# Kernel optimization log

Hardware: AMD Instinct MI355X
Metric: run time of the kernel (lower is better)

The kernel has to match this reference:

```python
import jax, jax.numpy as jnp
import numpy as np

EMBED_DIM = 1024
NUM_HEADS = 16
HEAD_DIM = EMBED_DIM // NUM_HEADS


def setup_inputs() -> dict:
    key = jax.random.key(0)
    ks = jax.random.split(key, 10)
    s = 1.0 / np.sqrt(EMBED_DIM)
    x = jax.random.normal(ks[0], (4, 2048, EMBED_DIM), dtype=jnp.float32)
    return {
        "x": x,
        "Wq": jax.random.normal(ks[1], (EMBED_DIM, EMBED_DIM), jnp.float32) * s,
        "bq": jnp.zeros((EMBED_DIM,), jnp.float32),
        "Wk": jax.random.normal(ks[2], (EMBED_DIM, EMBED_DIM), jnp.float32) * s,
        "bk": jnp.zeros((EMBED_DIM,), jnp.float32),
        "Wv": jax.random.normal(ks[3], (EMBED_DIM, EMBED_DIM), jnp.float32) * s,
        "bv": jnp.zeros((EMBED_DIM,), jnp.float32),
        "Wo": jax.random.normal(ks[4], (EMBED_DIM, EMBED_DIM), jnp.float32) * s,
        "bo": jnp.zeros((EMBED_DIM,), jnp.float32),
        "head_scaling": jnp.ones((NUM_HEADS,), jnp.float32),
    }


def reference(x, Wq, bq, Wk, bk, Wv, bv, Wo, bo, head_scaling):
    B, S, E = x.shape
    H, D = NUM_HEADS, HEAD_DIM
    scale = 1.0 / np.sqrt(D)
    # projections (torch Linear: y = x @ W.T + b)
    q = (x @ Wq.T + bq).reshape(B, S, H, D).transpose(0, 2, 1, 3)  # [B,H,S,D]
    k = (x @ Wk.T + bk).reshape(B, S, H, D).transpose(0, 2, 1, 3)
    v = (x @ Wv.T + bv).reshape(B, S, H, D).transpose(0, 2, 1, 3)
    scores = jnp.einsum("bhqd,bhkd->bhqk", q, k) * scale
    attn = jax.nn.softmax(scores, axis=-1)
    head_imp = jax.nn.softmax(head_scaling)[None, :, None, None]  # [1,H,1,1]
    attn = attn * head_imp
    out = jnp.einsum("bhqk,bhkd->bhqd", attn, v)
    out = out.transpose(0, 2, 1, 3).reshape(B, S, E)
    return out @ Wo.T + bo
```

## Files before the change

### kernel.cpp

```cpp
#include <hip/hip_runtime.h>

typedef __bf16 bf16x8 __attribute__((ext_vector_type(8)));
typedef float f32x4 __attribute__((ext_vector_type(4)));

constexpr int E = 1024;
constexpr int T = 8192;
constexpr size_t TE  = (size_t)T * E;
constexpr size_t WSZ = (size_t)E * E;

#define QSCALE 0.18033688011112042f

__device__ __forceinline__ unsigned short f2bf(float f) {
    union { float f; unsigned int i; } x; x.f = f;
    unsigned int i = x.i;
    return (unsigned short)((i + 0x7fffu + ((i >> 16) & 1u)) >> 16);
}

__device__ __forceinline__ unsigned int pack_rtz(float lo, float hi) {
    return __builtin_amdgcn_perm(
        __builtin_bit_cast(unsigned int, hi),
        __builtin_bit_cast(unsigned int, lo), 0x07060302u);
}

__device__ __forceinline__ void gload16(const unsigned short* g, unsigned short* l) {
    __builtin_amdgcn_global_load_lds(
        (const __attribute__((address_space(1))) unsigned int*)g,
        (__attribute__((address_space(3))) unsigned int*)l, 16, 0, 0);
}

__global__ __launch_bounds__(256)
void cvt_kernel(const float* __restrict__ x,
                const float* __restrict__ w0, const float* __restrict__ w1,
                const float* __restrict__ w2, const float* __restrict__ w3,
                unsigned short* __restrict__ xb, unsigned short* __restrict__ wb)
{
    size_t i = ((size_t)blockIdx.x * 256 + threadIdx.x) * 8;
    const float* src;
    unsigned short* dst;
    if (i < TE) { src = x + i; dst = xb + i; }
    else {
        size_t j = i - TE;
        int w = (int)(j >> 20);
        size_t off = j & (WSZ - 1);
        src = (w == 0 ? w0 : w == 1 ? w1 : w == 2 ? w2 : w3) + off;
        dst = wb + ((size_t)w << 20) + off;
    }
    float4 a = *(const float4*)src;
    float4 b = *(const float4*)(src + 4);
    union { unsigned short u[8]; uint4 v; } p;
    p.u[0] = f2bf(a.x); p.u[1] = f2bf(a.y); p.u[2] = f2bf(a.z); p.u[3] = f2bf(a.w);
    p.u[4] = f2bf(b.x); p.u[5] = f2bf(b.y); p.u[6] = f2bf(b.z); p.u[7] = f2bf(b.w);
    *(uint4*)dst = p.v;
}

template <int MODE>
__device__ __forceinline__ void gemm_body2(unsigned short* __restrict__ As,
                                           unsigned short* __restrict__ Bs,
                                           const unsigned short* __restrict__ X,
                                           const unsigned short* __restrict__ W,
                                           const float* __restrict__ bias,
                                           void* __restrict__ outp, int t0, int n0,
                                           float oscale)
{
    const int tid  = threadIdx.x;
    const int wave = tid >> 6;
    const int lane = tid & 63;
    const int quad = lane >> 4;
    const int l16  = lane & 15;
    const int wm   = wave >> 2;
    const int wn   = wave & 3;
    const int srow = tid >> 3;
    const int sch  = (tid & 7) ^ ((tid >> 4) & 7);
    const int fsw8 = (l16 >> 1) & 7;

    f32x4 acc[4][4];
#pragma unroll
    for (int i = 0; i < 4; i++)
#pragma unroll
        for (int j = 0; j < 4; j++)
            acc[i][j] = (f32x4){0.f, 0.f, 0.f, 0.f};

    for (int k0 = 0; k0 < E; k0 += 64) {
#pragma unroll
        for (int p = 0; p < 2; p++)
            gload16(&X[(size_t)(t0 + p * 64 + srow) * E + k0 + sch * 8], &As[p * 4096 + tid * 8]);
#pragma unroll
        for (int p = 0; p < 4; p++)
            gload16(&W[(size_t)(n0 + p * 64 + srow) * E + k0 + sch * 8], &Bs[p * 4096 + tid * 8]);
        __syncthreads();

#pragma unroll
        for (int ks = 0; ks < 2; ks++) {
            const int rch = ((ks * 4 + quad) ^ fsw8) * 8;
            bf16x8 af[4], bfr[4];
#pragma unroll
            for (int i = 0; i < 4; i++)
                af[i] = *(const bf16x8*)&As[(wm * 64 + i * 16 + l16) * 64 + rch];
#pragma unroll
            for (int j = 0; j < 4; j++)
                bfr[j] = *(const bf16x8*)&Bs[(wn * 64 + j * 16 + l16) * 64 + rch];

#pragma unroll
            for (int i = 0; i < 4; i++)
#pragma unroll
                for (int j = 0; j < 4; j++) {
                    if (MODE == 2)
                        acc[i][j] = __builtin_amdgcn_mfma_f32_16x16x32_bf16(af[i], bfr[j], acc[i][j], 0, 0, 0);
                    else
                        acc[i][j] = __builtin_amdgcn_mfma_f32_16x16x32_bf16(bfr[j], af[i], acc[i][j], 0, 0, 0);
                }
        }
        __syncthreads();
    }

    if (MODE == 2) {
#pragma unroll
        for (int j = 0; j < 4; j++) {
            const int gc = n0 + wn * 64 + j * 16 + l16;
            const float bj = bias[gc];
#pragma unroll
            for (int i = 0; i < 4; i++) {
                const int gr0 = t0 + wm * 64 + i * 16 + quad * 4;
                union { unsigned short u[4]; uint2 v; } o;
#pragma unroll
                for (int r = 0; r < 4; r++) o.u[r] = f2bf((acc[i][j][r] + bj) * oscale);
                unsigned short* vt = (unsigned short*)outp;
                *(uint2*)&vt[((size_t)((gr0 >> 11) * 16 + (gc >> 6)) * 64 + (gc & 63)) * 2048 + (gr0 & 2047)] = o.v;
            }
        }
    } else {
#pragma unroll
        for (int j = 0; j < 4; j++) {
            const int nb = n0 + wn * 64 + j * 16 + quad * 4;
            const float4 b4 = *(const float4*)&bias[nb];
#pragma unroll
            for (int i = 0; i < 4; i++) {
                const int t = t0 + wm * 64 + i * 16 + l16;
                union { unsigned short u[4]; uint2 v; } o;
                o.u[0] = f2bf((acc[i][j][0] + b4.x) * oscale);
                o.u[1] = f2bf((acc[i][j][1] + b4.y) * oscale);
                o.u[2] = f2bf((acc[i][j][2] + b4.z) * oscale);
                o.u[3] = f2bf((acc[i][j][3] + b4.w) * oscale);
                *(uint2*)&((unsigned short*)outp)[(size_t)t * E + nb] = o.v;
            }
        }
    }
}

__device__ __forceinline__ void gemm_body_out(const unsigned short* __restrict__ X,
                                              const unsigned short* __restrict__ W,
                                              const float* __restrict__ bias,
                                              float* __restrict__ outp, int t0, int n0)
{
    __shared__ unsigned short As[128 * 64];
    __shared__ unsigned short Bs[128 * 64];

    const int tid  = threadIdx.x;
    const int wave = tid >> 6;
    const int lane = tid & 63;
    const int quad = lane >> 4;
    const int l16  = lane & 15;
    const int wm   = wave >> 1;
    const int wn   = wave & 1;
    const int srow = tid >> 3;
    const int sch  = (tid & 7) ^ ((tid >> 4) & 7);
    const int fsw8 = (l16 >> 1) & 7;

    f32x4 acc[4][4];
#pragma unroll
    for (int i = 0; i < 4; i++)
#pragma unroll
        for (int j = 0; j < 4; j++)
            acc[i][j] = (f32x4){0.f, 0.f, 0.f, 0.f};

    for (int k0 = 0; k0 < E; k0 += 64) {
#pragma unroll
        for (int j = 0; j < 4; j++) {
            gload16(&X[(size_t)(t0 + j * 32 + srow) * E + k0 + sch * 8], &As[j * 2048 + tid * 8]);
            gload16(&W[(size_t)(n0 + j * 32 + srow) * E + k0 + sch * 8], &Bs[j * 2048 + tid * 8]);
        }
        __syncthreads();

#pragma unroll
        for (int ks = 0; ks < 2; ks++) {
            const int rch = ((ks * 4 + quad) ^ fsw8) * 8;
            bf16x8 af[4], bfr[4];
#pragma unroll
            for (int i = 0; i < 4; i++)
                af[i] = *(const bf16x8*)&As[(wm * 64 + i * 16 + l16) * 64 + rch];
#pragma unroll
            for (int j = 0; j < 4; j++)
                bfr[j] = *(const bf16x8*)&Bs[(wn * 64 + j * 16 + l16) * 64 + rch];

#pragma unroll
            for (int i = 0; i < 4; i++)
#pragma unroll
                for (int j = 0; j < 4; j++)
                    acc[i][j] = __builtin_amdgcn_mfma_f32_16x16x32_bf16(bfr[j], af[i], acc[i][j], 0, 0, 0);
        }
        __syncthreads();
    }

#pragma unroll
    for (int j = 0; j < 4; j++) {
        const int nb = n0 + wn * 64 + j * 16 + quad * 4;
        const float4 b4 = *(const float4*)&bias[nb];
#pragma unroll
        for (int i = 0; i < 4; i++) {
            const int t = t0 + wm * 64 + i * 16 + l16;
            float4 o;
            o.x = acc[i][j][0] + b4.x;
            o.y = acc[i][j][1] + b4.y;
            o.z = acc[i][j][2] + b4.z;
            o.w = acc[i][j][3] + b4.w;
            *(float4*)&outp[(size_t)t * E + nb] = o;
        }
    }
}

__global__ __launch_bounds__(512)
void gemm_qkv(const unsigned short* __restrict__ Xb, const unsigned short* __restrict__ Wb,
              const float* __restrict__ bq, const float* __restrict__ bk, const float* __restrict__ bv,
              unsigned short* __restrict__ Qb, unsigned short* __restrict__ Kb, unsigned short* __restrict__ VTb)
{
    __shared__ unsigned short smem[(128 + 256) * 64];
    unsigned short* As = smem;
    unsigned short* Bs = smem + 128 * 64;

    const int t0 = blockIdx.x * 128;
    const int y = blockIdx.y;
    const int seg = y >> 2;
    const int n0 = (y & 3) * 256;
    const unsigned short* W = Wb + (size_t)seg * WSZ;
    if (seg == 0)      gemm_body2<0>(As, Bs, Xb, W, bq, Qb,  t0, n0, QSCALE);
    else if (seg == 1) gemm_body2<0>(As, Bs, Xb, W, bk, Kb,  t0, n0, 1.0f);
    else               gemm_body2<2>(As, Bs, Xb, W, bv, VTb, t0, n0, 1.0f);
}

__global__ __launch_bounds__(256, 4)
void gemm_out(const unsigned short* __restrict__ AOb, const unsigned short* __restrict__ Wob,
              const float* __restrict__ bo, float* __restrict__ out)
{
    gemm_body_out(AOb, Wob, bo, out, blockIdx.x * 128, blockIdx.y * 128);
}

__global__ __launch_bounds__(256, 4)
void attn_kernel(const unsigned short* __restrict__ Q,
                 const unsigned short* __restrict__ K,
                 const unsigned short* __restrict__ VT,
                 const float* __restrict__ hs,
                 unsigned short* __restrict__ AO)
{
    constexpr int S = 2048, H = 16;
    const int hb = blockIdx.x;
    const int qt = blockIdx.y;
    const int h  = hb >> 2;
    const int b  = hb & 3;

    const int tid  = threadIdx.x;
    const int wave = tid >> 6;
    const int lane = tid & 63;
    const int quad = lane >> 4;
    const int l16  = lane & 15;

    __shared__ unsigned short Kpl[2][2 * 64 * 32];
    __shared__ unsigned short Vpl[2][64 * 64];

    float mx = -1e30f;
    for (int i = 0; i < H; i++) mx = fmaxf(mx, hs[i]);
    float ss = 0.f;
    for (int i = 0; i < H; i++) ss += __expf(hs[i] - mx);
    const float head_imp = __expf(hs[h] - mx) / ss;

    const int base_t  = b * S;
    const int colbase = h * 64;
    const int q0 = qt * 128 + wave * 32;

    bf16x8 qf[2][2];
#pragma unroll
    for (int qi = 0; qi < 2; qi++)
#pragma unroll
        for (int c = 0; c < 2; c++)
            qf[qi][c] = *(const bf16x8*)&Q[(size_t)(base_t + q0 + qi * 16 + l16) * E + colbase + c * 32 + quad * 8];

    union { unsigned short u[8]; bf16x8 v; } onesf;
    {
        const unsigned short ov = (l16 == 0) ? (unsigned short)0x3F80 : (unsigned short)0;
#pragma unroll
        for (int j = 0; j < 8; j++) onesf.u[j] = ov;
    }

    f32x4 oT[2][4];
#pragma unroll
    for (int qi = 0; qi < 2; qi++)
#pragma unroll
        for (int t = 0; t < 4; t++) oT[qi][t] = (f32x4){0.f, 0.f, 0.f, 0.f};
    f32x4 oT5[2];
    oT5[0] = (f32x4){0.f, 0.f, 0.f, 0.f};
    oT5[1] = (f32x4){0.f, 0.f, 0.f, 0.f};

    const int ksc  = (tid & 3) ^ ((tid >> 3) & 3);
    const int vsc  = (tid & 7) ^ ((tid >> 4) & 7);
    const int fsw  = (l16 >> 1) & 3;
    const int fsw8 = (l16 >> 1) & 7;
    const unsigned short* const vbase = VT + (size_t)(b * 16 + h) * 64 * 2048;

    const unsigned short* kg = &K[(size_t)(base_t + (tid >> 2)) * E + colbase + ksc * 8];
    const unsigned short* vg = &vbase[(size_t)(tid >> 3) * 2048 + vsc * 8];

    auto stage = [&](int bu) {
#pragma unroll
        for (int j = 0; j < 2; j++)
            gload16(kg + j * 32, &Kpl[bu][j * 2048 + tid * 8]);
#pragma unroll
        for (int j = 0; j < 2; j++)
            gload16(vg + (size_t)j * 32 * 2048, &Vpl[bu][j * 2048 + tid * 8]);
        kg += 64 * E;
        vg += 64;
    };

    stage(0);

#pragma unroll 2
    for (int kt = 0; kt < 32; kt++) {
        __syncthreads();
        if (kt < 31) stage((kt + 1) & 1);
        const int cb = kt & 1;

        union { unsigned int w[4]; bf16x8 v; } pb[2][2];
#pragma unroll
        for (int ks = 0; ks < 2; ks++) {
            unsigned int pw[2][4];
#pragma unroll
            for (int tkl = 0; tkl < 2; tkl++) {
                const int tk = ks * 2 + tkl;
                const int ko = (tk * 16 + l16) * 32 + (quad ^ fsw) * 8;
                bf16x8 kf0 = *(const bf16x8*)&Kpl[cb][ko];
                bf16x8 kf1 = *(const bf16x8*)&Kpl[cb][2048 + ko];
#pragma unroll
                for (int qi = 0; qi < 2; qi++) {
                    f32x4 st = (f32x4){0.f, 0.f, 0.f, 0.f};
                    st = __builtin_amdgcn_mfma_f32_16x16x32_bf16(kf0, qf[qi][0], st, 0, 0, 0);
                    st = __builtin_amdgcn_mfma_f32_16x16x32_bf16(kf1, qf[qi][1], st, 0, 0, 0);
                    float p0 = __builtin_amdgcn_exp2f(st[0]);
                    float p1 = __builtin_amdgcn_exp2f(st[1]);
                    float p2 = __builtin_amdgcn_exp2f(st[2]);
                    float p3 = __builtin_amdgcn_exp2f(st[3]);
                    pw[qi][tkl * 2 + 0] = pack_rtz(p0, p1);
                    pw[qi][tkl * 2 + 1] = pack_rtz(p2, p3);
                }
            }
#pragma unroll
            for (int qi = 0; qi < 2; qi++) {
                auto s1 = __builtin_amdgcn_permlane32_swap(pw[qi][0], pw[qi][2], false, false);
                auto s2 = __builtin_amdgcn_permlane32_swap(pw[qi][1], pw[qi][3], false, false);
                auto t1 = __builtin_amdgcn_permlane16_swap(s1[0], s1[1], false, false);
                auto t2 = __builtin_amdgcn_permlane16_swap(s2[0], s2[1], false, false);
                pb[qi][ks].w[0] = t1[0];
                pb[qi][ks].w[1] = t2[0];
                pb[qi][ks].w[2] = t1[1];
                pb[qi][ks].w[3] = t2[1];
            }
        }

        __builtin_amdgcn_s_setprio(1);
#pragma unroll
        for (int tau = 0; tau < 4; tau++) {
#pragma unroll
            for (int ks = 0; ks < 2; ks++) {
                bf16x8 vf = *(const bf16x8*)&Vpl[cb][(tau * 16 + l16) * 64 + ((ks * 4 + quad) ^ fsw8) * 8];
#pragma unroll
                for (int qi = 0; qi < 2; qi++)
                    oT[qi][tau] = __builtin_amdgcn_mfma_f32_16x16x32_bf16(vf, pb[qi][ks].v, oT[qi][tau], 0, 0, 0);
            }
        }
#pragma unroll
        for (int qi = 0; qi < 2; qi++)
#pragma unroll
            for (int ks = 0; ks < 2; ks++)
                oT5[qi] = __builtin_amdgcn_mfma_f32_16x16x32_bf16(onesf.v, pb[qi][ks].v, oT5[qi], 0, 0, 0);
        __builtin_amdgcn_s_setprio(0);
    }

#pragma unroll
    for (int qi = 0; qi < 2; qi++) {
        const float l = __shfl(oT5[qi][0], l16);
        const float inv = head_imp / l;
#pragma unroll
        for (int tau = 0; tau < 4; tau++) {
            union { unsigned short u[4]; uint2 v; } o;
#pragma unroll
            for (int r = 0; r < 4; r++) o.u[r] = f2bf(oT[qi][tau][r] * inv);
            *(uint2*)&AO[(size_t)(base_t + q0 + qi * 16 + l16) * E + colbase + tau * 16 + quad * 4] = o.v;
        }
    }
}

extern "C" void kernel_launch(void* const* d_in, const int* in_sizes, int n_in,
                              void* d_out, int out_size, void* d_ws, size_t ws_size,
                              hipStream_t stream)
{
    const float* x  = (const float*)d_in[0];
    const float* Wq = (const float*)d_in[1];
    const float* bq = (const float*)d_in[2];
    const float* Wk = (const float*)d_in[3];
    const float* bk = (const float*)d_in[4];
    const float* Wv = (const float*)d_in[5];
    const float* bv = (const float*)d_in[6];
    const float* Wo = (const float*)d_in[7];
    const float* bo = (const float*)d_in[8];
    const float* hs = (const float*)d_in[9];
    float* out = (float*)d_out;

    unsigned short* ws = (unsigned short*)d_ws;
    unsigned short* xb  = ws;
    unsigned short* wb  = ws + TE;
    unsigned short* Qb  = ws + TE + 4 * WSZ;
    unsigned short* AOb = Qb + TE;

    unsigned short* Kb;
    unsigned short* VTb;
    const size_t need_bytes = (5 * TE + 4 * WSZ) * sizeof(unsigned short);
    if (ws_size >= need_bytes) {
        Kb  = AOb + TE;
        VTb = Kb + TE;
    } else {
        Kb  = (unsigned short*)d_out;
        VTb = Kb + TE;
    }

    hipLaunchKernelGGL(cvt_kernel, dim3(6144, 1, 1), dim3(256, 1, 1), 0, stream, x, Wq, Wk, Wv, Wo, xb, wb);
    hipLaunchKernelGGL(gemm_qkv, dim3(64, 12, 1), dim3(512, 1, 1), 0, stream, xb, wb, bq, bk, bv, Qb, Kb, VTb);
    hipLaunchKernelGGL(attn_kernel, dim3(64, 16, 1), dim3(256, 1, 1), 0, stream, Qb, Kb, VTb, hs, AOb);
    hipLaunchKernelGGL(gemm_out, dim3(64, 8, 1), dim3(256, 1, 1), 0, stream, AOb, wb + 3 * WSZ, bo, out);
}
```

Before: 258.0 us.

## Double-buffer GEMM LDS tiles with K-step 32 and one barrier per iteration

Both projection GEMMs (QKV and output) now use two LDS buffers holding 32-wide K tiles instead of one 64-wide tile. The next tile's global-to-LDS load is issued right after a single barrier, so it overlaps with the MFMA work on the current buffer, and the second barrier per iteration is gone. The swizzle is rewritten for the 4-chunk rows. Trade-offs are twice as many loop iterations with fewer MFMAs per barrier, and a different LDS footprint that may affect occupancy.

```diff
diff --git a/kernel.cpp b/kernel.cpp
--- a/kernel.cpp
+++ b/kernel.cpp
@@ -54,8 +54,7 @@
 }
 
 template <int MODE>
-__device__ __forceinline__ void gemm_body2(unsigned short* __restrict__ As,
-                                           unsigned short* __restrict__ Bs,
+__device__ __forceinline__ void gemm_body2(unsigned short* __restrict__ smem,
                                            const unsigned short* __restrict__ X,
                                            const unsigned short* __restrict__ W,
                                            const float* __restrict__ bias,
@@ -69,9 +68,8 @@
     const int l16  = lane & 15;
     const int wm   = wave >> 2;
     const int wn   = wave & 3;
-    const int srow = tid >> 3;
-    const int sch  = (tid & 7) ^ ((tid >> 4) & 7);
-    const int fsw8 = (l16 >> 1) & 7;
+    const int gc   = (tid & 3) ^ ((tid >> 3) & 3);
+    const int fsw  = (l16 >> 1) & 3;
 
     f32x4 acc[4][4];
 #pragma unroll
@@ -80,44 +78,50 @@
         for (int j = 0; j < 4; j++)
             acc[i][j] = (f32x4){0.f, 0.f, 0.f, 0.f};
 
-    for (int k0 = 0; k0 < E; k0 += 64) {
-#pragma unroll
-        for (int p = 0; p < 2; p++)
-            gload16(&X[(size_t)(t0 + p * 64 + srow) * E + k0 + sch * 8], &As[p * 4096 + tid * 8]);
-#pragma unroll
-        for (int p = 0; p < 4; p++)
-            gload16(&W[(size_t)(n0 + p * 64 + srow) * E + k0 + sch * 8], &Bs[p * 4096 + tid * 8]);
+    const unsigned short* xg = &X[(size_t)(t0 + (tid >> 2)) * E + gc * 8];
+    const unsigned short* wg = &W[(size_t)(n0 + (tid >> 2)) * E + gc * 8];
+
+    auto stage = [&](int bu) {
+        unsigned short* buf = smem + bu * 12288;
+        gload16(xg, &buf[tid * 8]);
+        gload16(wg, &buf[4096 + tid * 8]);
+        gload16(wg + (size_t)128 * E, &buf[8192 + tid * 8]);
+        xg += 32; wg += 32;
+    };
+
+    stage(0);
+
+#pragma unroll 2
+    for (int kt = 0; kt < 32; kt++) {
         __syncthreads();
-
-#pragma unroll
-        for (int ks = 0; ks < 2; ks++) {
-            const int rch = ((ks * 4 + quad) ^ fsw8) * 8;
-            bf16x8 af[4], bfr[4];
-#pragma unroll
-            for (int i = 0; i < 4; i++)
-                af[i] = *(const bf16x8*)&As[(wm * 64 + i * 16 + l16) * 64 + rch];
-#pragma unroll
-            for (int j = 0; j < 4; j++)
-                bfr[j] = *(const bf16x8*)&Bs[(wn * 64 + j * 16 + l16) * 64 + rch];
-
-#pragma unroll
-            for (int i = 0; i < 4; i++)
-#pragma unroll
-                for (int j = 0; j < 4; j++) {
-                    if (MODE == 2)
-                        acc[i][j] = __builtin_amdgcn_mfma_f32_16x16x32_bf16(af[i], bfr[j], acc[i][j], 0, 0, 0);
-                    else
-                        acc[i][j] = __builtin_amdgcn_mfma_f32_16x16x32_bf16(bfr[j], af[i], acc[i][j], 0, 0, 0);
-                }
-        }
-        __syncthreads();
+        if (kt < 31) stage((kt + 1) & 1);
+        const unsigned short* As = smem + (kt & 1) * 12288;
+        const unsigned short* Bs = As + 4096;
+
+        bf16x8 af[4], bfr[4];
+#pragma unroll
+        for (int i = 0; i < 4; i++)
+            af[i] = *(const bf16x8*)&As[(wm * 64 + i * 16 + l16) * 32 + (quad ^ fsw) * 8];
+#pragma unroll
+        for (int j = 0; j < 4; j++)
+            bfr[j] = *(const bf16x8*)&Bs[(wn * 64 + j * 16 + l16) * 32 + (quad ^ fsw) * 8];
+
+#pragma unroll
+        for (int i = 0; i < 4; i++)
+#pragma unroll
+            for (int j = 0; j < 4; j++) {
+                if (MODE == 2)
+                    acc[i][j] = __builtin_amdgcn_mfma_f32_16x16x32_bf16(af[i], bfr[j], acc[i][j], 0, 0, 0);
+                else
+                    acc[i][j] = __builtin_amdgcn_mfma_f32_16x16x32_bf16(bfr[j], af[i], acc[i][j], 0, 0, 0);
+            }
     }
 
     if (MODE == 2) {
 #pragma unroll
         for (int j = 0; j < 4; j++) {
-            const int gc = n0 + wn * 64 + j * 16 + l16;
-            const float bj = bias[gc];
+            const int gcn = n0 + wn * 64 + j * 16 + l16;
+            const float bj = bias[gcn];
 #pragma unroll
             for (int i = 0; i < 4; i++) {
                 const int gr0 = t0 + wm * 64 + i * 16 + quad * 4;
@@ -125,7 +129,7 @@
 #pragma unroll
                 for (int r = 0; r < 4; r++) o.u[r] = f2bf((acc[i][j][r] + bj) * oscale);
                 unsigned short* vt = (unsigned short*)outp;
-                *(uint2*)&vt[((size_t)((gr0 >> 11) * 16 + (gc >> 6)) * 64 + (gc & 63)) * 2048 + (gr0 & 2047)] = o.v;
+                *(uint2*)&vt[((size_t)((gr0 >> 11) * 16 + (gcn >> 6)) * 64 + (gcn & 63)) * 2048 + (gr0 & 2047)] = o.v;
             }
         }
     } else {
@@ -152,8 +156,7 @@
                                               const float* __restrict__ bias,
                                               float* __restrict__ outp, int t0, int n0)
 {
-    __shared__ unsigned short As[128 * 64];
-    __shared__ unsigned short Bs[128 * 64];
+    __shared__ unsigned short smem[2 * (128 + 128) * 32];
 
     const int tid  = threadIdx.x;
     const int wave = tid >> 6;
@@ -162,9 +165,8 @@
     const int l16  = lane & 15;
     const int wm   = wave >> 1;
     const int wn   = wave & 1;
-    const int srow = tid >> 3;
-    const int sch  = (tid & 7) ^ ((tid >> 4) & 7);
-    const int fsw8 = (l16 >> 1) & 7;
+    const int gc   = (tid & 3) ^ ((tid >> 3) & 3);
+    const int fsw  = (l16 >> 1) & 3;
 
     f32x4 acc[4][4];
 #pragma unroll
@@ -173,32 +175,40 @@
         for (int j = 0; j < 4; j++)
             acc[i][j] = (f32x4){0.f, 0.f, 0.f, 0.f};
 
-    for (int k0 = 0; k0 < E; k0 += 64) {
-#pragma unroll
-        for (int j = 0; j < 4; j++) {
-            gload16(&X[(size_t)(t0 + j * 32 + srow) * E + k0 + sch * 8], &As[j * 2048 + tid * 8]);
-            gload16(&W[(size_t)(n0 + j * 32 + srow) * E + k0 + sch * 8], &Bs[j * 2048 + tid * 8]);
-        }
+    const unsigned short* xg = &X[(size_t)(t0 + (tid >> 2)) * E + gc * 8];
+    const unsigned short* wg = &W[(size_t)(n0 + (tid >> 2)) * E + gc * 8];
+
+    auto stage = [&](int bu) {
+        unsigned short* buf = smem + bu * 8192;
+        gload16(xg, &buf[tid * 8]);
+        gload16(xg + (size_t)64 * E, &buf[2048 + tid * 8]);
+        gload16(wg, &buf[4096 + tid * 8]);
+        gload16(wg + (size_t)64 * E, &buf[6144 + tid * 8]);
+        xg += 32; wg += 32;
+    };
+
+    stage(0);
+
+#pragma unroll 2
+    for (int kt = 0; kt < 32; kt++) {
         __syncthreads();
-
-#pragma unroll
-        for (int ks = 0; ks < 2; ks++) {
-            const int rch = ((ks * 4 + quad) ^ fsw8) * 8;
-            bf16x8 af[4], bfr[4];
-#pragma unroll
-            for (int i = 0; i < 4; i++)
-                af[i] = *(const bf16x8*)&As[(wm * 64 + i * 16 + l16) * 64 + rch];
+        if (kt < 31) stage((kt + 1) & 1);
+        const unsigned short* As = smem + (kt & 1) * 8192;
+        const unsigned short* Bs = As + 4096;
+
+        bf16x8 af[4], bfr[4];
+#pragma unroll
+        for (int i = 0; i < 4; i++)
+            af[i] = *(const bf16x8*)&As[(wm * 64 + i * 16 + l16) * 32 + (quad ^ fsw) * 8];
+#pragma unroll
+        for (int j = 0; j < 4; j++)
+            bfr[j] = *(const bf16x8*)&Bs[(wn * 64 + j * 16 + l16) * 32 + (quad ^ fsw) * 8];
+
+#pragma unroll
+        for (int i = 0; i < 4; i++)
 #pragma unroll
             for (int j = 0; j < 4; j++)
-                bfr[j] = *(const bf16x8*)&Bs[(wn * 64 + j * 16 + l16) * 64 + rch];
-
-#pragma unroll
-            for (int i = 0; i < 4; i++)
-#pragma unroll
-                for (int j = 0; j < 4; j++)
-                    acc[i][j] = __builtin_amdgcn_mfma_f32_16x16x32_bf16(bfr[j], af[i], acc[i][j], 0, 0, 0);
-        }
-        __syncthreads();
+                acc[i][j] = __builtin_amdgcn_mfma_f32_16x16x32_bf16(bfr[j], af[i], acc[i][j], 0, 0, 0);
     }
 
 #pragma unroll
@@ -223,18 +233,16 @@
               const float* __restrict__ bq, const float* __restrict__ bk, const float* __restrict__ bv,
               unsigned short* __restrict__ Qb, unsigned short* __restrict__ Kb, unsigned short* __restrict__ VTb)
 {
-    __shared__ unsigned short smem[(128 + 256) * 64];
-    unsigned short* As = smem;
-    unsigned short* Bs = smem + 128 * 64;
+    __shared__ unsigned short smem[2 * (128 + 256) * 32];
 
     const int t0 = blockIdx.x * 128;
     const int y = blockIdx.y;
     const int seg = y >> 2;
     const int n0 = (y & 3) * 256;
     const unsigned short* W = Wb + (size_t)seg * WSZ;
-    if (seg == 0)      gemm_body2<0>(As, Bs, Xb, W, bq, Qb,  t0, n0, QSCALE);
-    else if (seg == 1) gemm_body2<0>(As, Bs, Xb, W, bk, Kb,  t0, n0, 1.0f);
-    else               gemm_body2<2>(As, Bs, Xb, W, bv, VTb, t0, n0, 1.0f);
+    if (seg == 0)      gemm_body2<0>(smem, Xb, W, bq, Qb,  t0, n0, QSCALE);
+    else if (seg == 1) gemm_body2<0>(smem, Xb, W, bk, Kb,  t0, n0, 1.0f);
+    else               gemm_body2<2>(smem, Xb, W, bv, VTb, t0, n0, 1.0f);
 }
 
 __global__ __launch_bounds__(256, 4)
```

Measured after the change: 265.5 us. 1.03x slower.
